# Performance work log

Hardware: AMD Instinct MI355X
Metric: run time of the kernel (lower is better)

## Reference

```python
import jax, jax.numpy as jnp
import numpy as np

B, T, D = 1, 2048, 1024
E, DFF = 8, 4096


def setup_inputs() -> dict:
    key = jax.random.key(0)
    k1, k2, k3, k4 = jax.random.split(key, 4)
    x = jax.random.normal(k1, (B, T, D), dtype=jnp.float32)
    Wg = jax.random.normal(k2, (D, E), dtype=jnp.float32) * (1.0 / np.sqrt(D))
    w1 = jax.random.normal(k3, (D, DFF), dtype=jnp.float32) * (1.0 / np.sqrt(D))
    w2 = jax.random.normal(k4, (DFF, D), dtype=jnp.float32) * (1.0 / np.sqrt(DFF))
    return {"x": x, "Wg": Wg, "w1": w1, "w2": w2}


def _gating(logits):
    # logits: [S, E]; capacity = S (per source code)
    S, num_e = logits.shape
    gates = jax.nn.softmax(logits.astype(jnp.float32), axis=1)  # [S,E] fp32
    idx1 = jnp.argmax(gates, axis=1)                            # top-1 expert
    mask1 = jax.nn.one_hot(idx1, num_e, dtype=jnp.int32)        # [S,E]
    logits_ex1 = jnp.where(mask1.astype(bool), -jnp.inf, logits)
    idx2 = jnp.argmax(logits_ex1, axis=1)                       # top-2 expert
    mask2 = jax.nn.one_hot(idx2, num_e, dtype=jnp.int32)
    # slot position of each token inside its expert buffer
    loc1 = jnp.cumsum(mask1, axis=0) - 1                        # [S,E]
    loc2 = jnp.cumsum(mask2, axis=0) - 1 + jnp.sum(mask1, axis=0, keepdims=True)
    loc1_s = jnp.sum(loc1 * mask1, axis=1)                      # [S] int
    loc2_s = jnp.sum(loc2 * mask2, axis=1)
    g1 = jnp.sum(gates * mask1, axis=1)                         # [S]
    g2 = jnp.sum(gates * mask2, axis=1)
    denom = jnp.maximum(g1 + g2, jnp.finfo(jnp.float32).eps)
    g1, g2 = g1 / denom, g2 / denom
    cap = S
    loc1_sc = jax.nn.one_hot(loc1_s, cap, dtype=jnp.float32)    # [S,C]
    loc2_sc = jax.nn.one_hot(loc2_s, cap, dtype=jnp.float32)
    # combine_weights: [S,E,C]
    combine = (g1[:, None] * mask1)[:, :, None] * loc1_sc[:, None, :] \
            + (g2[:, None] * mask2)[:, :, None] * loc2_sc[:, None, :]
    dispatch_mask = combine != 0
    return combine.astype(logits.dtype), dispatch_mask


def reference(x, Wg, w1, w2):
    d_model = x.shape[2]
    xs = x.reshape(-1, d_model)                                  # [S,D]
    logits = xs @ Wg                                             # gate linear
    combine, dispatch_mask = _gating(logits)
    # one-hot scatter dispatch: [S,E,C] x [S,D] -> [E,C,D]
    dispatched = jnp.einsum('sec,sm->ecm', dispatch_mask.astype(jnp.float32), xs)
    # all-to-all is an identity permutation of the expert dim in single-process ref
    expert_out = jax.nn.relu(dispatched @ w1) @ w2               # [E,C,D]
    # one-hot gather combine: [S,E,C] x [E,C,D] -> [S,D]
    out = jnp.einsum('sec,ecm->sm', combine, expert_out)
    return out.reshape(x.shape)
```

## Files before the change

### kernel.cpp

```cpp
#include <hip/hip_runtime.h>
#include <stdint.h>


typedef __attribute__((ext_vector_type(4))) float f32x4;
typedef __attribute__((ext_vector_type(8))) short bf16x8;

#define GPTR(p) (const __attribute__((address_space(1))) void*)(p)
#define LPTR(p) (__attribute__((address_space(3))) void*)(p)

__device__ __forceinline__ ushort f2bf(float f) {
  uint32_t u = __float_as_uint(f);
  uint32_t r = (u + 0x7FFFu + ((u >> 16) & 1u)) >> 16;
  return (ushort)r;
}
__device__ __forceinline__ float bf2f(ushort u) {
  return __uint_as_float((uint32_t)u << 16);
}

__global__ void cvt4(const float* __restrict__ in, ushort* __restrict__ out, int n4) {
  int i = blockIdx.x * blockDim.x + threadIdx.x;
  if (i >= n4) return;
  float4 v = ((const float4*)in)[i];
  ushort4 o;
  o.x = f2bf(v.x); o.y = f2bf(v.y); o.z = f2bf(v.z); o.w = f2bf(v.w);
  ((ushort4*)out)[i] = o;
}

__global__ void transpose_cvt(const float* __restrict__ in, ushort* __restrict__ out,
                              int R, int C) {
  __shared__ float tile[32][33];
  const int c0 = blockIdx.x * 32, r0 = blockIdx.y * 32;
  const int tx = threadIdx.x, ty = threadIdx.y;
#pragma unroll
  for (int i = 0; i < 32; i += 8)
    tile[ty + i][tx] = in[(size_t)(r0 + ty + i) * C + (c0 + tx)];
  __syncthreads();
#pragma unroll
  for (int i = 0; i < 32; i += 8)
    out[(size_t)(c0 + ty + i) * R + (r0 + tx)] = f2bf(tile[tx][ty + i]);
}

__global__ void reduce_out(float* __restrict__ out, const ushort* __restrict__ pb,
                           int SD) {
  int i = blockIdx.x * blockDim.x + threadIdx.x;
  if (i >= SD / 4) return;
  f32x4 a = ((const f32x4*)out)[i];
#pragma unroll
  for (int j = 0; j < 3; ++j) {
    ushort4 u = ((const ushort4*)(pb + (size_t)j * SD))[i];
    a[0] += bf2f(u.x); a[1] += bf2f(u.y); a[2] += bf2f(u.z); a[3] += bf2f(u.w);
  }
  ((f32x4*)out)[i] = a;
}

template <int MODE>
__global__ __launch_bounds__(512) void gemm_pipe(const ushort* __restrict__ A,
                                                 const ushort* __restrict__ Bt,
                                                 void* __restrict__ C0,
                                                 void* __restrict__ C1,
                                                 int M, int N, int Ks, int Ktot,
                                                 int nx, int ny) {
  constexpr int BM = 128, BN = 256, BK = 64;
  __shared__ ushort As[3][BM * BK];
  __shared__ ushort Bs[3][BN * BK];

  const int tid = threadIdx.x;
  const int lane = tid & 63, wid = tid >> 6;
  const int wr = wid >> 2, wc = wid & 3;

  const int cpx = gridDim.x >> 3;
  const int swz = (blockIdx.x & 7) * cpx + (blockIdx.x >> 3);
  const int bx = swz % nx;
  const int by = (swz / nx) % ny;
  const int bz = swz / (nx * ny);
  const int row0 = by * BM, col0 = bx * BN;
  const int kbase = bz * Ks;

  f32x4 acc[4][4];
#pragma unroll
  for (int m = 0; m < 4; ++m)
#pragma unroll
    for (int n = 0; n < 4; ++n) acc[m][n] = (f32x4){0.f, 0.f, 0.f, 0.f};

  const int rA = tid >> 3;
  const int cb = (tid & 7) * 16;
  auto stage = [&](int buf, int k0) {
#pragma unroll
    for (int i = 0; i < 2; ++i) {
      int r = i * 64 + rA;
      int csw = cb ^ ((r & 7) << 4);
      __builtin_amdgcn_global_load_lds(
          GPTR((const char*)(A + (size_t)(row0 + r) * Ktot + k0) + csw),
          LPTR((char*)&As[buf][0] + i * 8192 + wid * 1024), 16, 0, 0);
    }
#pragma unroll
    for (int j = 0; j < 4; ++j) {
      int r = j * 64 + rA;
      int csw = cb ^ ((r & 7) << 4);
      __builtin_amdgcn_global_load_lds(
          GPTR((const char*)(Bt + (size_t)(col0 + r) * Ktot + k0) + csw),
          LPTR((char*)&Bs[buf][0] + j * 8192 + wid * 1024), 16, 0, 0);
    }
  };

  const int nt = Ks / BK;
  stage(0, kbase);
  stage(1, kbase + BK);

  for (int t = 0; t < nt; ++t) {
    if (t < nt - 1) asm volatile("s_waitcnt vmcnt(6)" ::: "memory");
    else            asm volatile("s_waitcnt vmcnt(0)" ::: "memory");
    __builtin_amdgcn_sched_barrier(0);
    __builtin_amdgcn_s_barrier();
    __builtin_amdgcn_sched_barrier(0);
    if (t + 2 < nt) stage((t + 2) % 3, kbase + (size_t)(t + 2) * BK);

    const ushort* Ab = As[t % 3];
    const ushort* Bb = Bs[t % 3];
#pragma unroll
    for (int kk = 0; kk < 2; ++kk) {
      const int kb2 = kk * 64 + (lane >> 4) * 16;
      bf16x8 a[4], b[4];
#pragma unroll
      for (int m = 0; m < 4; ++m) {
        int R = wr * 64 + m * 16 + (lane & 15);
        a[m] = *(const bf16x8*)((const char*)Ab + R * 128 + (kb2 ^ ((R & 7) << 4)));
      }
#pragma unroll
      for (int n = 0; n < 4; ++n) {
        int R = wc * 64 + n * 16 + (lane & 15);
        b[n] = *(const bf16x8*)((const char*)Bb + R * 128 + (kb2 ^ ((R & 7) << 4)));
      }
      __builtin_amdgcn_s_setprio(1);
#pragma unroll
      for (int m = 0; m < 4; ++m)
#pragma unroll
        for (int n = 0; n < 4; ++n)
          acc[m][n] = __builtin_amdgcn_mfma_f32_16x16x32_bf16(a[m], b[n], acc[m][n], 0, 0, 0);
      __builtin_amdgcn_s_setprio(0);
    }
  }

  const int rbase = row0 + wr * 64, cbase = col0 + wc * 64;
#pragma unroll
  for (int m = 0; m < 4; ++m) {
#pragma unroll
    for (int n = 0; n < 4; ++n) {
      const int col = cbase + n * 16 + (lane & 15);
      const int r0q = rbase + m * 16 + ((lane >> 4) << 2);
#pragma unroll
      for (int j = 0; j < 4; ++j) {
        float v = acc[m][n][j];
        size_t idx = (size_t)(r0q + j) * N + col;
        if (MODE == 1) {
          v = v > 0.f ? v : 0.f;
          ((ushort*)C0)[idx] = f2bf(v);
        } else {
          if (bz == 0)
            ((float*)C0)[idx] = v;
          else
            ((ushort*)C1)[(size_t)(bz - 1) * M * N + idx] = f2bf(v);
        }
      }
    }
  }
}

extern "C" void kernel_launch(void* const* d_in, const int* in_sizes, int n_in,
                              void* d_out, int out_size, void* d_ws, size_t ws_size,
                              hipStream_t stream) {
  const float* x  = (const float*)d_in[0];
  const float* w1 = (const float*)d_in[2];
  const float* w2 = (const float*)d_in[3];
  float* out = (float*)d_out;

  constexpr int S = 2048, D = 1024, F = 4096;
  char* ws = (char*)d_ws;
  ushort* xb  = (ushort*)(ws);
  ushort* w1t = (ushort*)(ws + (size_t)S * D * 2);
  ushort* w2t = (ushort*)(ws + (size_t)(S * D + F * D) * 2);
  ushort* H   = (ushort*)(ws + (size_t)(S * D + 2 * F * D) * 2);
  ushort* pb = (ushort*)(ws);

  hipLaunchKernelGGL(cvt4, dim3((S * D / 4 + 255) / 256), dim3(256), 0, stream,
                     x, xb, S * D / 4);
  hipLaunchKernelGGL(transpose_cvt, dim3(F / 32, D / 32), dim3(32, 8), 0, stream,
                     w1, w1t, D, F);
  hipLaunchKernelGGL(transpose_cvt, dim3(D / 32, F / 32), dim3(32, 8), 0, stream,
                     w2, w2t, F, D);
  hipLaunchKernelGGL((gemm_pipe<1>), dim3(256), dim3(512), 0, stream,
                     xb, w1t, (void*)H, nullptr, S, F, D, D, F / 256, S / 128);
  hipLaunchKernelGGL((gemm_pipe<2>), dim3(256), dim3(512), 0, stream,
                     H, w2t, (void*)out, (void*)pb, S, D, F / 4, F, D / 256, S / 128);
  hipLaunchKernelGGL(reduce_out, dim3((S * D / 4 + 255) / 256), dim3(256), 0, stream,
                     out, pb, S * D);
}
```

Measured before the change: 79.89 us.

## Fuse prep kernels, switch to 32x32x16 MFMA, remap block-to-XCD tiling

The three conversion/transpose kernels become one prep kernel, which saves two launches. The GEMM inner loop moves from 16x16x32 MFMA to 32x32x16 MFMA with 2x2 accumulators per wave, so each wave issues fewer LDS reads per MFMA. Block indices are remapped so the blocks on each XCD (blockIdx & 7) cover a contiguous 4x8 tile region or K-chunk for better L2 locality. This risks LDS bank conflicts with the new 32-lane read pattern and a changed epilogue store pattern.

```diff
diff --git a/kernel.cpp b/kernel.cpp
--- a/kernel.cpp
+++ b/kernel.cpp
@@ -3,6 +3,7 @@
 
 
 typedef __attribute__((ext_vector_type(4))) float f32x4;
+typedef __attribute__((ext_vector_type(16))) float f32x16;
 typedef __attribute__((ext_vector_type(8))) short bf16x8;
 
 #define GPTR(p) (const __attribute__((address_space(1))) void*)(p)
@@ -17,20 +18,12 @@
   return __uint_as_float((uint32_t)u << 16);
 }
 
-__global__ void cvt4(const float* __restrict__ in, ushort* __restrict__ out, int n4) {
-  int i = blockIdx.x * blockDim.x + threadIdx.x;
-  if (i >= n4) return;
-  float4 v = ((const float4*)in)[i];
-  ushort4 o;
-  o.x = f2bf(v.x); o.y = f2bf(v.y); o.z = f2bf(v.z); o.w = f2bf(v.w);
-  ((ushort4*)out)[i] = o;
-}
-
-__global__ void transpose_cvt(const float* __restrict__ in, ushort* __restrict__ out,
-                              int R, int C) {
+__device__ __forceinline__ void tile_transpose(const float* __restrict__ in,
+                                               ushort* __restrict__ out,
+                                               int R, int C, int bx, int by,
+                                               int tx, int ty) {
   __shared__ float tile[32][33];
-  const int c0 = blockIdx.x * 32, r0 = blockIdx.y * 32;
-  const int tx = threadIdx.x, ty = threadIdx.y;
+  const int c0 = bx * 32, r0 = by * 32;
 #pragma unroll
   for (int i = 0; i < 32; i += 8)
     tile[ty + i][tx] = in[(size_t)(r0 + ty + i) * C + (c0 + tx)];
@@ -38,6 +31,26 @@
 #pragma unroll
   for (int i = 0; i < 32; i += 8)
     out[(size_t)(c0 + ty + i) * R + (r0 + tx)] = f2bf(tile[tx][ty + i]);
+}
+
+__global__ void prep(const float* __restrict__ x, const float* __restrict__ w1,
+                     const float* __restrict__ w2, ushort* __restrict__ xb,
+                     ushort* __restrict__ w1t, ushort* __restrict__ w2t) {
+  const int b = blockIdx.x;
+  const int tx = threadIdx.x, ty = threadIdx.y;
+  if (b < 2048) {
+    int i = b * 256 + ty * 32 + tx;
+    float4 v = ((const float4*)x)[i];
+    ushort4 o;
+    o.x = f2bf(v.x); o.y = f2bf(v.y); o.z = f2bf(v.z); o.w = f2bf(v.w);
+    ((ushort4*)xb)[i] = o;
+  } else if (b < 6144) {
+    int b2 = b - 2048;
+    tile_transpose(w1, w1t, 1024, 4096, b2 & 127, b2 >> 7, tx, ty);
+  } else {
+    int b3 = b - 6144;
+    tile_transpose(w2, w2t, 4096, 1024, b3 & 31, b3 >> 5, tx, ty);
+  }
 }
 
 __global__ void reduce_out(float* __restrict__ out, const ushort* __restrict__ pb,
@@ -59,7 +72,7 @@
                                                  void* __restrict__ C0,
                                                  void* __restrict__ C1,
                                                  int M, int N, int Ks, int Ktot,
-                                                 int nx, int ny) {
+                                                 int ncx, int cpz) {
   constexpr int BM = 128, BN = 256, BK = 64;
   __shared__ ushort As[3][BM * BK];
   __shared__ ushort Bs[3][BN * BK];
@@ -68,19 +81,20 @@
   const int lane = tid & 63, wid = tid >> 6;
   const int wr = wid >> 2, wc = wid & 3;
 
-  const int cpx = gridDim.x >> 3;
-  const int swz = (blockIdx.x & 7) * cpx + (blockIdx.x >> 3);
-  const int bx = swz % nx;
-  const int by = (swz / nx) % ny;
-  const int bz = swz / (nx * ny);
+  const int ck = blockIdx.x & 7;
+  const int w = blockIdx.x >> 3;
+  const int bz = ck / cpz;
+  const int rem = ck % cpz;
+  const int bx = (rem % ncx) * 4 + (w & 3);
+  const int by = (rem / ncx) * 8 + (w >> 2);
   const int row0 = by * BM, col0 = bx * BN;
   const int kbase = bz * Ks;
 
-  f32x4 acc[4][4];
-#pragma unroll
-  for (int m = 0; m < 4; ++m)
-#pragma unroll
-    for (int n = 0; n < 4; ++n) acc[m][n] = (f32x4){0.f, 0.f, 0.f, 0.f};
+  f32x16 acc[2][2];
+#pragma unroll
+  for (int m = 0; m < 2; ++m)
+#pragma unroll
+    for (int n = 0; n < 2; ++n) acc[m][n] = (f32x16)(0.f);
 
   const int rA = tid >> 3;
   const int cb = (tid & 7) * 16;
@@ -118,40 +132,40 @@
     const ushort* Ab = As[t % 3];
     const ushort* Bb = Bs[t % 3];
 #pragma unroll
-    for (int kk = 0; kk < 2; ++kk) {
-      const int kb2 = kk * 64 + (lane >> 4) * 16;
-      bf16x8 a[4], b[4];
-#pragma unroll
-      for (int m = 0; m < 4; ++m) {
-        int R = wr * 64 + m * 16 + (lane & 15);
+    for (int s = 0; s < 4; ++s) {
+      const int kb2 = s * 32 + (lane >> 5) * 16;
+      bf16x8 a[2], b[2];
+#pragma unroll
+      for (int m = 0; m < 2; ++m) {
+        int R = wr * 64 + m * 32 + (lane & 31);
         a[m] = *(const bf16x8*)((const char*)Ab + R * 128 + (kb2 ^ ((R & 7) << 4)));
       }
 #pragma unroll
-      for (int n = 0; n < 4; ++n) {
-        int R = wc * 64 + n * 16 + (lane & 15);
+      for (int n = 0; n < 2; ++n) {
+        int R = wc * 64 + n * 32 + (lane & 31);
         b[n] = *(const bf16x8*)((const char*)Bb + R * 128 + (kb2 ^ ((R & 7) << 4)));
       }
       __builtin_amdgcn_s_setprio(1);
 #pragma unroll
-      for (int m = 0; m < 4; ++m)
-#pragma unroll
-        for (int n = 0; n < 4; ++n)
-          acc[m][n] = __builtin_amdgcn_mfma_f32_16x16x32_bf16(a[m], b[n], acc[m][n], 0, 0, 0);
+      for (int m = 0; m < 2; ++m)
+#pragma unroll
+        for (int n = 0; n < 2; ++n)
+          acc[m][n] = __builtin_amdgcn_mfma_f32_32x32x16_bf16(a[m], b[n], acc[m][n], 0, 0, 0);
       __builtin_amdgcn_s_setprio(0);
     }
   }
 
   const int rbase = row0 + wr * 64, cbase = col0 + wc * 64;
 #pragma unroll
-  for (int m = 0; m < 4; ++m) {
-#pragma unroll
-    for (int n = 0; n < 4; ++n) {
-      const int col = cbase + n * 16 + (lane & 15);
-      const int r0q = rbase + m * 16 + ((lane >> 4) << 2);
-#pragma unroll
-      for (int j = 0; j < 4; ++j) {
-        float v = acc[m][n][j];
-        size_t idx = (size_t)(r0q + j) * N + col;
+  for (int m = 0; m < 2; ++m) {
+#pragma unroll
+    for (int n = 0; n < 2; ++n) {
+      const int col = cbase + n * 32 + (lane & 31);
+#pragma unroll
+      for (int r = 0; r < 16; ++r) {
+        const int row = rbase + m * 32 + (r & 3) + 8 * (r >> 2) + 4 * (lane >> 5);
+        float v = acc[m][n][r];
+        size_t idx = (size_t)row * N + col;
         if (MODE == 1) {
           v = v > 0.f ? v : 0.f;
           ((ushort*)C0)[idx] = f2bf(v);
@@ -182,16 +196,12 @@
   ushort* H   = (ushort*)(ws + (size_t)(S * D + 2 * F * D) * 2);
   ushort* pb = (ushort*)(ws);
 
-  hipLaunchKernelGGL(cvt4, dim3((S * D / 4 + 255) / 256), dim3(256), 0, stream,
-                     x, xb, S * D / 4);
-  hipLaunchKernelGGL(transpose_cvt, dim3(F / 32, D / 32), dim3(32, 8), 0, stream,
-                     w1, w1t, D, F);
-  hipLaunchKernelGGL(transpose_cvt, dim3(D / 32, F / 32), dim3(32, 8), 0, stream,
-                     w2, w2t, F, D);
+  hipLaunchKernelGGL(prep, dim3(10240), dim3(32, 8), 0, stream,
+                     x, w1, w2, xb, w1t, w2t);
   hipLaunchKernelGGL((gemm_pipe<1>), dim3(256), dim3(512), 0, stream,
-                     xb, w1t, (void*)H, nullptr, S, F, D, D, F / 256, S / 128);
+                     xb, w1t, (void*)H, nullptr, S, F, D, D, 4, 8);
   hipLaunchKernelGGL((gemm_pipe<2>), dim3(256), dim3(512), 0, stream,
-                     H, w2t, (void*)out, (void*)pb, S, D, F / 4, F, D / 256, S / 128);
+                     H, w2t, (void*)out, (void*)pb, S, D, F / 4, F, 1, 2);
   hipLaunchKernelGGL(reduce_out, dim3((S * D / 4 + 255) / 256), dim3(256), 0, stream,
                      out, pb, S * D);
 }
```

Result: faster. 74.90 us (-6.3%).
